# Kernel tuning notes

Hardware: AMD Instinct MI355X
Metric: run time of the kernel (lower is better)

Reference implementation:

```python
import jax, jax.numpy as jnp
import numpy as np

B, S, IN, E, H, FF, L = 8, 1024, 128, 512, 8, 2048, 4
HD = E // H
EPS = 1e-5


def make_pe(seq_len, d_model):
    position = np.arange(seq_len, dtype=np.float32)[:, None]
    div_term = np.exp(np.arange(0, d_model, 2, dtype=np.float32) * (-np.log(10000.0) / d_model))
    pe = np.zeros((seq_len, d_model), dtype=np.float32)
    pe[:, 0::2] = np.sin(position * div_term)
    pe[:, 1::2] = np.cos(position * div_term)
    return jnp.asarray(pe)


def setup_inputs() -> dict:
    key = jax.random.key(0)
    ks = jax.random.split(key, 16)
    s = 0.02
    return {
        "src": jax.random.normal(ks[0], (B, S, IN), jnp.float32),
        "distances": jax.random.uniform(ks[1], (B, S, S), jnp.float32),
        "proj_w": jax.random.normal(ks[2], (E, IN), jnp.float32) * s,
        "proj_b": jnp.zeros((E,), jnp.float32),
        "bn_g": jnp.ones((E,), jnp.float32),
        "bn_b": jnp.zeros((E,), jnp.float32),
        "in_proj_w": jax.random.normal(ks[3], (3 * E, E), jnp.float32) * s,
        "in_proj_b": jnp.zeros((3 * E,), jnp.float32),
        "dist_scale": jnp.array(1.0, jnp.float32),
        "lin1_w": jax.random.normal(ks[4], (FF, E), jnp.float32) * s,
        "lin1_b": jnp.zeros((FF,), jnp.float32),
        "lin2_w": jax.random.normal(ks[5], (E, FF), jnp.float32) * s,
        "lin2_b": jnp.zeros((E,), jnp.float32),
        "n1_g": jnp.ones((E,), jnp.float32),
        "n1_b": jnp.zeros((E,), jnp.float32),
        "n2_g": jnp.ones((E,), jnp.float32),
        "n2_b": jnp.zeros((E,), jnp.float32),
    }


def layernorm(x, g, b):
    m = jnp.mean(x, axis=-1, keepdims=True)
    v = jnp.var(x, axis=-1, keepdims=True)
    return (x - m) * jax.lax.rsqrt(v + EPS) * g + b


def reference(src, distances, proj_w, proj_b, bn_g, bn_b, in_proj_w, in_proj_b,
              dist_scale, lin1_w, lin1_b, lin2_w, lin2_b, n1_g, n1_b, n2_g, n2_b):
    # input projection
    x = jnp.einsum('bsi,ei->bse', src, proj_w) + proj_b  # [B,S,E]
    # BatchNorm1d over flattened (B*S) dim, training-mode batch stats
    xf = x.reshape(-1, E)
    mu = jnp.mean(xf, axis=0)
    var = jnp.var(xf, axis=0)
    x = ((xf - mu) * jax.lax.rsqrt(var + EPS) * bn_g + bn_b).reshape(B, S, E)
    # positional encoding
    x = x + make_pe(S, E)[None]
    # distance bias (same for every layer)
    dmax = jnp.max(distances, axis=-1, keepdims=True)
    dist_bias = jnp.exp(dist_scale * (1.0 - distances / dmax))  # [B,S,S]
    scale = 1.0 / jnp.sqrt(jnp.float32(HD))
    # num_layers iterations of the SAME (shared-parameter) layer
    for _ in range(L):
        qkv = jnp.einsum('bse,fe->bsf', x, in_proj_w) + in_proj_b  # [B,S,3E]
        q, k, v = jnp.split(qkv, 3, axis=-1)
        q = q.reshape(B, S, H, HD).transpose(0, 2, 1, 3)
        k = k.reshape(B, S, H, HD).transpose(0, 2, 1, 3)
        scores = jnp.einsum('bhqd,bhkd->bhqk', q, k) * scale  # [B,H,S,S]
        attn = jax.nn.softmax(scores, axis=-1)
        avg_w = jnp.mean(attn, axis=1)  # head-averaged weights [B,S,S]
        w = avg_w * dist_bias
        w = w / jnp.sum(w, axis=-1, keepdims=True)
        # NOTE: original bmm uses raw layer input as value (no V/out projection)
        attn_out = jnp.einsum('bqk,bke->bqe', w, x)
        x = layernorm(x + attn_out, n1_g, n1_b)
        ff = jnp.einsum('bsf,ef->bse', jax.nn.relu(jnp.einsum('bse,fe->bsf', x, lin1_w) + lin1_b), lin2_w) + lin2_b
        x = layernorm(x + ff, n2_g, n2_b)
    return x
```

## Files before the change

kernel.cpp:

```cpp
#include <hip/hip_runtime.h>
#include <hip/hip_bf16.h>
#include <math.h>

#define Bz 8
#define Sz 1024
#define INz 128
#define Ez 512
#define Hz 8
#define HDz 64
#define FFz 2048
#define Lz 4
#define Nz (Bz*Sz)
#define EPSf 1e-5f

typedef __attribute__((ext_vector_type(8))) short short8;
typedef __attribute__((ext_vector_type(4))) float floatx4;
#define MFMA16(a,b,c) __builtin_amdgcn_mfma_f32_16x16x32_bf16(a,b,c,0,0,0)

typedef __hip_bfloat16 bf16;

__device__ inline float b2f(bf16 v) { return __bfloat162float(v); }
__device__ inline bf16 f2b(float v) { return __float2bfloat16(v); }

__device__ inline void gload16(const bf16* g, bf16* lds_base)
{
  __builtin_amdgcn_global_load_lds(
      (const __attribute__((address_space(1))) void*)g,
      (__attribute__((address_space(3))) void*)lds_base,
      16, 0, 0);
}

__global__ __launch_bounds__(256) void cast_f2b(const float* __restrict__ in,
    bf16* __restrict__ out, int n)
{
  int i = blockIdx.x * 256 + threadIdx.x;
  if (i < n) out[i] = f2b(in[i]);
}

__global__ __launch_bounds__(256) void gemm_bt(
    const bf16* __restrict__ A, const bf16* __restrict__ Wm,
    const float* __restrict__ bias, float* __restrict__ Cf,
    bf16* __restrict__ Cb, const float* __restrict__ rowscale,
    int M, int N, int K, long sA, long sW, long sC, int relu)
{
  int z = blockIdx.z;
  A  += (size_t)z * sA;
  Wm += (size_t)z * sW;
  if (rowscale) rowscale += (size_t)z * M;
  size_t cbase = (size_t)z * sC;
  int bm = blockIdx.y * 128, bn = blockIdx.x * 128;
  __shared__ __align__(16) bf16 As[128][64];
  __shared__ __align__(16) bf16 Bs[128][64];
  int t = threadIdx.x, wave = t >> 6, lane = t & 63;
  int wm = (wave >> 1) * 64, wn = (wave & 1) * 64;
  int fr = lane & 15, fo = (lane >> 4) * 8;
  int srow = lane >> 3, scol = (lane & 7) * 8;
  floatx4 acc[4][4];
  #pragma unroll
  for (int i = 0; i < 4; ++i)
    #pragma unroll
    for (int j = 0; j < 4; ++j) acc[i][j] = (floatx4){0.f, 0.f, 0.f, 0.f};

  for (int k0 = 0; k0 < K; k0 += 64) {
    #pragma unroll
    for (int i = 0; i < 4; ++i) {
      int chunk = wave * 4 + i;
      int row = chunk * 8 + srow;
      gload16(A  + (size_t)(bm + row) * K + k0 + scol, &As[chunk * 8][0]);
      gload16(Wm + (size_t)(bn + row) * K + k0 + scol, &Bs[chunk * 8][0]);
    }
    __syncthreads();
    #pragma unroll
    for (int ks = 0; ks < 2; ++ks) {
      short8 af[4], bfv[4];
      #pragma unroll
      for (int rt = 0; rt < 4; ++rt) af[rt]  = *(const short8*)&As[wm + rt * 16 + fr][ks * 32 + fo];
      #pragma unroll
      for (int ct = 0; ct < 4; ++ct) bfv[ct] = *(const short8*)&Bs[wn + ct * 16 + fr][ks * 32 + fo];
      #pragma unroll
      for (int rt = 0; rt < 4; ++rt)
        #pragma unroll
        for (int ct = 0; ct < 4; ++ct)
          acc[rt][ct] = MFMA16(af[rt], bfv[ct], acc[rt][ct]);
    }
    __syncthreads();
  }
  #pragma unroll
  for (int rt = 0; rt < 4; ++rt) {
    #pragma unroll
    for (int r = 0; r < 4; ++r) {
      int row = bm + wm + rt * 16 + (lane >> 4) * 4 + r;
      float rs = rowscale ? (1.f / rowscale[row]) : 1.f;
      #pragma unroll
      for (int ct = 0; ct < 4; ++ct) {
        int col = bn + wn + ct * 16 + fr;
        float v = acc[rt][ct][r] + (bias ? bias[col] : 0.f);
        if (relu) v = fmaxf(v, 0.f);
        v *= rs;
        if (Cf) Cf[cbase + (size_t)row * N + col] = v;
        if (Cb) Cb[cbase + (size_t)row * N + col] = f2b(v);
      }
    }
  }
}

__global__ __launch_bounds__(256) void bn_stats(const float* __restrict__ x, float* __restrict__ st)
{
  int c = blockIdx.x;
  float s = 0.f, q = 0.f;
  for (int r = threadIdx.x; r < Nz; r += 256) {
    float v = x[(size_t)r * Ez + c];
    s += v; q += v * v;
  }
  for (int o = 32; o; o >>= 1) { s += __shfl_down(s, o); q += __shfl_down(q, o); }
  __shared__ float shs[4], shq[4];
  int w = threadIdx.x >> 6;
  if ((threadIdx.x & 63) == 0) { shs[w] = s; shq[w] = q; }
  __syncthreads();
  if (threadIdx.x == 0) {
    s = shs[0] + shs[1] + shs[2] + shs[3];
    q = shq[0] + shq[1] + shq[2] + shq[3];
    float mu = s / (float)Nz;
    float var = q / (float)Nz - mu * mu;
    st[c] = mu;
    st[Ez + c] = rsqrtf(var + EPSf);
  }
}

__global__ __launch_bounds__(256) void bn_apply_pe(const float* __restrict__ x0,
    const float* __restrict__ st, const float* __restrict__ g,
    const float* __restrict__ b, float* __restrict__ x, bf16* __restrict__ xb)
{
  int idx = blockIdx.x * 256 + threadIdx.x;
  int c = idx & (Ez - 1);
  int r = idx >> 9;
  int s = r & (Sz - 1);
  float dt = expf((float)(c & ~1) * (-9.210340371976184f / (float)Ez));
  float ang = (float)s * dt;
  float pe = (c & 1) ? cosf(ang) : sinf(ang);
  float mu = st[c], rs = st[Ez + c];
  float v = (x0[idx] - mu) * rs * g[c] + b[c] + pe;
  x[idx] = v;
  xb[idx] = f2b(v);
}

__global__ __launch_bounds__(256) void dist_bias_k(const float* __restrict__ dist,
    const float* __restrict__ dsc, bf16* __restrict__ db)
{
  size_t base = (size_t)blockIdx.x * Sz;
  float m = -1e30f;
  for (int j = threadIdx.x; j < Sz; j += 256) m = fmaxf(m, dist[base + j]);
  for (int o = 32; o; o >>= 1) m = fmaxf(m, __shfl_down(m, o));
  __shared__ float sh[4];
  if ((threadIdx.x & 63) == 0) sh[threadIdx.x >> 6] = m;
  __syncthreads();
  m = fmaxf(fmaxf(sh[0], sh[1]), fmaxf(sh[2], sh[3]));
  float sc = dsc[0];
  float inv = 1.f / m;
  for (int j = threadIdx.x; j < Sz; j += 256)
    db[base + j] = f2b(expf(sc * (1.f - dist[base + j] * inv)));
}

__global__ __launch_bounds__(256) void transpose_xb(const bf16* __restrict__ xb,
    bf16* __restrict__ xT)
{
  int b = blockIdx.z, e0 = blockIdx.y * 32, s0 = blockIdx.x * 32;
  __shared__ bf16 T[32][40];
  int t = threadIdx.x, row = t >> 3, c = t & 7;
  *(ushort4*)&T[row][c * 4] = *(const ushort4*)(xb + (size_t)(b * Sz + s0 + row) * Ez + e0 + c * 4);
  __syncthreads();
  ushort4 v;
  unsigned short* vp = (unsigned short*)&v;
  #pragma unroll
  for (int i = 0; i < 4; ++i) vp[i] = *(const unsigned short*)&T[c * 4 + i][row];
  *(ushort4*)(xT + ((size_t)b * Ez + e0 + row) * Sz + s0 + c * 4) = v;
}

__global__ __launch_bounds__(256) void attn_stats2(const bf16* __restrict__ qk,
    float* __restrict__ stats)
{
  int qt = blockIdx.x, h = blockIdx.y, b = blockIdx.z;
  int q0 = qt * 64;
  __shared__ bf16 Qs[64][72];
  __shared__ bf16 Ks[128][72];
  int t = threadIdx.x, wave = t >> 6, lane = t & 63;
  int fr = lane & 15, fo = (lane >> 4) * 8;
  #pragma unroll
  for (int i = 0; i < 2; ++i) {
    int idx = i * 256 + t, row = idx >> 3, c4 = idx & 7;
    *(float4*)&Qs[row][c4 * 8] =
      *(const float4*)(qk + (size_t)(b * Sz + q0 + row) * 1024 + h * 64 + c4 * 8);
  }
  __syncthreads();
  short8 aq0 = *(const short8*)&Qs[wave * 16 + fr][fo];
  short8 aq1 = *(const short8*)&Qs[wave * 16 + fr][32 + fo];
  float m_run[4] = {-1e30f, -1e30f, -1e30f, -1e30f};
  float z_run[4] = {0.f, 0.f, 0.f, 0.f};
  for (int k0 = 0; k0 < Sz; k0 += 128) {
    __syncthreads();
    #pragma unroll
    for (int i = 0; i < 4; ++i) {
      int idx = i * 256 + t, row = idx >> 3, c4 = idx & 7;
      *(float4*)&Ks[row][c4 * 8] =
        *(const float4*)(qk + (size_t)(b * Sz + k0 + row) * 1024 + 512 + h * 64 + c4 * 8);
    }
    __syncthreads();
    float sc[8][4];
    #pragma unroll
    for (int j = 0; j < 8; ++j) {
      floatx4 a4 = (floatx4){0.f, 0.f, 0.f, 0.f};
      short8 b0 = *(const short8*)&Ks[j * 16 + fr][fo];
      short8 b1 = *(const short8*)&Ks[j * 16 + fr][32 + fo];
      a4 = MFMA16(aq0, b0, a4);
      a4 = MFMA16(aq1, b1, a4);
      #pragma unroll
      for (int r = 0; r < 4; ++r) sc[j][r] = a4[r] * 0.125f;
    }
    #pragma unroll
    for (int r = 0; r < 4; ++r) {
      float vm = sc[0][r];
      #pragma unroll
      for (int j = 1; j < 8; ++j) vm = fmaxf(vm, sc[j][r]);
      #pragma unroll
      for (int o = 1; o < 16; o <<= 1) vm = fmaxf(vm, __shfl_xor(vm, o, 16));
      float mn = fmaxf(m_run[r], vm);
      float zb = 0.f;
      #pragma unroll
      for (int j = 0; j < 8; ++j) zb += __expf(sc[j][r] - mn);
      #pragma unroll
      for (int o = 1; o < 16; o <<= 1) zb += __shfl_xor(zb, o, 16);
      z_run[r] = z_run[r] * __expf(m_run[r] - mn) + zb;
      m_run[r] = mn;
    }
  }
  if (fr == 0) {
    int qb = q0 + wave * 16 + (lane >> 4) * 4;
    #pragma unroll
    for (int r = 0; r < 4; ++r) {
      size_t o = ((size_t)(b * Hz + h) * Sz + qb + r) * 2;
      stats[o] = m_run[r];
      stats[o + 1] = z_run[r];
    }
  }
}

__global__ __launch_bounds__(256) void scores_bias(const bf16* __restrict__ qk,
    const bf16* __restrict__ db, const float* __restrict__ stats,
    bf16* __restrict__ aw)
{
  int kt = blockIdx.x, qt = blockIdx.y, b = blockIdx.z;
  int q0 = qt * 128, k0 = kt * 128;
  __shared__ bf16 Qs[128][72];
  __shared__ bf16 Ks[128][72];
  __shared__ float mS[128][9];
  __shared__ float ziS[128][9];
  int t = threadIdx.x, wave = t >> 6, lane = t & 63;
  int fr = lane & 15, fo = (lane >> 4) * 8;
  int wm = (wave >> 1) * 64, wn = (wave & 1) * 64;

  #pragma unroll
  for (int i = 0; i < 4; ++i) {
    int lin = i * 256 + t, h = lin >> 7, q = lin & 127;
    const float* sp = stats + ((size_t)(b * Hz + h) * Sz + q0 + q) * 2;
    mS[q][h] = sp[0];
    ziS[q][h] = 1.f / sp[1];
  }

  floatx4 pac[4][4];
  #pragma unroll
  for (int i = 0; i < 4; ++i)
    #pragma unroll
    for (int j = 0; j < 4; ++j) pac[i][j] = (floatx4){0.f, 0.f, 0.f, 0.f};

  for (int h = 0; h < 8; ++h) {
    __syncthreads();
    #pragma unroll
    for (int i = 0; i < 4; ++i) {
      int idx = i * 256 + t, row = idx >> 3, c4 = idx & 7;
      *(float4*)&Qs[row][c4 * 8] =
        *(const float4*)(qk + (size_t)(b * Sz + q0 + row) * 1024 + h * 64 + c4 * 8);
      *(float4*)&Ks[row][c4 * 8] =
        *(const float4*)(qk + (size_t)(b * Sz + k0 + row) * 1024 + 512 + h * 64 + c4 * 8);
    }
    __syncthreads();
    short8 bfv0[4], bfv1[4];
    #pragma unroll
    for (int ct = 0; ct < 4; ++ct) {
      bfv0[ct] = *(const short8*)&Ks[wn + ct * 16 + fr][fo];
      bfv1[ct] = *(const short8*)&Ks[wn + ct * 16 + fr][32 + fo];
    }
    #pragma unroll
    for (int rt = 0; rt < 4; ++rt) {
      short8 af0 = *(const short8*)&Qs[wm + rt * 16 + fr][fo];
      short8 af1 = *(const short8*)&Qs[wm + rt * 16 + fr][32 + fo];
      floatx4 sc[4];
      #pragma unroll
      for (int ct = 0; ct < 4; ++ct) {
        floatx4 z4 = (floatx4){0.f, 0.f, 0.f, 0.f};
        z4 = MFMA16(af0, bfv0[ct], z4);
        sc[ct] = MFMA16(af1, bfv1[ct], z4);
      }
      #pragma unroll
      for (int r = 0; r < 4; ++r) {
        int qloc = wm + rt * 16 + (lane >> 4) * 4 + r;
        float m = mS[qloc][h], zi = ziS[qloc][h];
        #pragma unroll
        for (int ct = 0; ct < 4; ++ct)
          pac[rt][ct][r] += __expf(sc[ct][r] * 0.125f - m) * zi;
      }
    }
  }

  #pragma unroll
  for (int rt = 0; rt < 4; ++rt) {
    #pragma unroll
    for (int r = 0; r < 4; ++r) {
      int qloc = wm + rt * 16 + (lane >> 4) * 4 + r;
      size_t rowoff = (size_t)(b * Sz + q0 + qloc) * Sz + k0;
      #pragma unroll
      for (int ct = 0; ct < 4; ++ct) {
        int kloc = wn + ct * 16 + fr;
        float p = pac[rt][ct][r] * 0.125f * b2f(db[rowoff + kloc]);
        aw[rowoff + kloc] = f2b(p);
      }
    }
  }
}

__global__ __launch_bounds__(256) void rowsum(const bf16* __restrict__ aw,
    float* __restrict__ den)
{
  size_t base = (size_t)blockIdx.x * Sz;
  int t = threadIdx.x;
  ushort4 u = *(const ushort4*)(aw + base + t * 4);
  float s = __uint_as_float((unsigned)u.x << 16) + __uint_as_float((unsigned)u.y << 16)
          + __uint_as_float((unsigned)u.z << 16) + __uint_as_float((unsigned)u.w << 16);
  for (int o = 32; o; o >>= 1) s += __shfl_down(s, o);
  __shared__ float sh[4];
  if ((t & 63) == 0) sh[t >> 6] = s;
  __syncthreads();
  if (t == 0) den[blockIdx.x] = sh[0] + sh[1] + sh[2] + sh[3];
}

__global__ __launch_bounds__(256) void add_ln(const float* __restrict__ xin,
    const float* __restrict__ dly, const float* __restrict__ g,
    const float* __restrict__ bb, float* __restrict__ xout, bf16* __restrict__ xbout)
{
  size_t base = (size_t)blockIdx.x * Ez;
  int t = threadIdx.x;
  float a0 = xin[base + t] + dly[base + t];
  float a1 = xin[base + t + 256] + dly[base + t + 256];
  float s = a0 + a1, q = a0 * a0 + a1 * a1;
  for (int o = 32; o; o >>= 1) { s += __shfl_down(s, o); q += __shfl_down(q, o); }
  __shared__ float shs[4], shq[4];
  if ((t & 63) == 0) { shs[t >> 6] = s; shq[t >> 6] = q; }
  __syncthreads();
  s = shs[0] + shs[1] + shs[2] + shs[3];
  q = shq[0] + shq[1] + shq[2] + shq[3];
  float mu = s * (1.f / Ez);
  float var = q * (1.f / Ez) - mu * mu;
  float rs = rsqrtf(var + EPSf);
  float v0 = (a0 - mu) * rs * g[t] + bb[t];
  float v1 = (a1 - mu) * rs * g[t + 256] + bb[t + 256];
  xout[base + t] = v0;
  xout[base + t + 256] = v1;
  xbout[base + t] = f2b(v0);
  xbout[base + t + 256] = f2b(v1);
}

extern "C" void kernel_launch(void* const* d_in, const int* in_sizes, int n_in,
                              void* d_out, int out_size, void* d_ws, size_t ws_size,
                              hipStream_t stream)
{
  const float* src        = (const float*)d_in[0];
  const float* distances  = (const float*)d_in[1];
  const float* proj_w     = (const float*)d_in[2];
  const float* proj_b     = (const float*)d_in[3];
  const float* bn_g       = (const float*)d_in[4];
  const float* bn_b       = (const float*)d_in[5];
  const float* in_proj_w  = (const float*)d_in[6];
  const float* in_proj_b  = (const float*)d_in[7];
  const float* dist_scale = (const float*)d_in[8];
  const float* lin1_w     = (const float*)d_in[9];
  const float* lin1_b     = (const float*)d_in[10];
  const float* lin2_w     = (const float*)d_in[11];
  const float* lin2_b     = (const float*)d_in[12];
  const float* n1_g       = (const float*)d_in[13];
  const float* n1_b       = (const float*)d_in[14];
  const float* n2_g       = (const float*)d_in[15];
  const float* n2_b       = (const float*)d_in[16];

  float* x = (float*)d_out;

  float* stats = (float*)d_ws;
  float* den   = stats + 131072;
  float* bnst  = den + 8192;
  float* aout  = bnst + 1024;
  float* x0    = aout;
  bf16* db_b = (bf16*)(aout + (size_t)Nz * Ez);
  bf16* Rqk  = db_b + (size_t)Bz * Sz * Sz;
  bf16* qk   = Rqk;
  bf16* aw   = Rqk + (size_t)Nz * 1024;
  bf16* ff1  = Rqk;
  bf16* xb   = Rqk + (size_t)Nz * FFz;
  bf16* xT   = xb + (size_t)Nz * Ez;
  bf16* srcb = xT + (size_t)Bz * Ez * Sz;
  bf16* wpr  = srcb + (size_t)Nz * INz;
  bf16* wqk  = wpr + Ez * INz;
  bf16* wl1  = wqk + 1024 * Ez;
  bf16* wl2  = wl1 + FFz * Ez;

  cast_f2b<<<(Nz * INz) / 256, 256, 0, stream>>>(src, srcb, Nz * INz);
  cast_f2b<<<(Ez * INz + 255) / 256, 256, 0, stream>>>(proj_w, wpr, Ez * INz);
  cast_f2b<<<(1024 * Ez) / 256, 256, 0, stream>>>(in_proj_w, wqk, 1024 * Ez);
  cast_f2b<<<(FFz * Ez) / 256, 256, 0, stream>>>(lin1_w, wl1, FFz * Ez);
  cast_f2b<<<(Ez * FFz) / 256, 256, 0, stream>>>(lin2_w, wl2, Ez * FFz);

  gemm_bt<<<dim3(Ez / 128, Nz / 128, 1), 256, 0, stream>>>(
      srcb, wpr, proj_b, x0, nullptr, nullptr, Nz, Ez, INz, 0, 0, 0, 0);
  bn_stats<<<Ez, 256, 0, stream>>>(x0, bnst);
  bn_apply_pe<<<(Nz * Ez) / 256, 256, 0, stream>>>(x0, bnst, bn_g, bn_b, x, xb);
  dist_bias_k<<<Bz * Sz, 256, 0, stream>>>(distances, dist_scale, db_b);

  for (int l = 0; l < Lz; ++l) {
    transpose_xb<<<dim3(Sz / 32, Ez / 32, Bz), 256, 0, stream>>>(xb, xT);
    gemm_bt<<<dim3(1024 / 128, Nz / 128, 1), 256, 0, stream>>>(
        xb, wqk, in_proj_b, nullptr, qk, nullptr, Nz, 1024, Ez, 0, 0, 0, 0);
    attn_stats2<<<dim3(Sz / 64, Hz, Bz), 256, 0, stream>>>(qk, stats);
    scores_bias<<<dim3(Sz / 128, Sz / 128, Bz), 256, 0, stream>>>(qk, db_b, stats, aw);
    rowsum<<<Bz * Sz, 256, 0, stream>>>(aw, den);
    gemm_bt<<<dim3(Ez / 128, Sz / 128, Bz), 256, 0, stream>>>(
        aw, xT, nullptr, aout, nullptr, den,
        Sz, Ez, Sz, (long)Sz * Sz, (long)Ez * Sz, (long)Sz * Ez, 0);
    add_ln<<<Nz, 256, 0, stream>>>(x, aout, n1_g, n1_b, x, xb);
    gemm_bt<<<dim3(FFz / 128, Nz / 128, 1), 256, 0, stream>>>(
        xb, wl1, lin1_b, nullptr, ff1, nullptr, Nz, FFz, Ez, 0, 0, 0, 1);
    gemm_bt<<<dim3(Ez / 128, Nz / 128, 1), 256, 0, stream>>>(
        ff1, wl2, lin2_b, aout, nullptr, nullptr, Nz, Ez, FFz, 0, 0, 0, 0);
    add_ln<<<Nz, 256, 0, stream>>>(x, aout, n2_g, n2_b, x, xb);
  }
}
```

Before: 1.282 ms.

## Double-buffer LDS tiles and XOR-swizzle layout in bf16 GEMM

The GEMM kernel now uses two LDS buffers, so the global-to-LDS load of the next K tile is issued before computing on the current one. This halves the barriers per K step and hides load latency. It also XOR-swizzles the 16-byte column chunks in LDS, both on store and on fragment read, to reduce bank conflicts. LDS use doubles to 64KB per block, which may lower occupancy.

```diff
diff --git a/kernel.cpp b/kernel.cpp
--- a/kernel.cpp
+++ b/kernel.cpp
@@ -49,42 +49,61 @@
   if (rowscale) rowscale += (size_t)z * M;
   size_t cbase = (size_t)z * sC;
   int bm = blockIdx.y * 128, bn = blockIdx.x * 128;
-  __shared__ __align__(16) bf16 As[128][64];
-  __shared__ __align__(16) bf16 Bs[128][64];
+  __shared__ __align__(16) bf16 As0[128][64], Bs0[128][64];
+  __shared__ __align__(16) bf16 As1[128][64], Bs1[128][64];
   int t = threadIdx.x, wave = t >> 6, lane = t & 63;
   int wm = (wave >> 1) * 64, wn = (wave & 1) * 64;
-  int fr = lane & 15, fo = (lane >> 4) * 8;
-  int srow = lane >> 3, scol = (lane & 7) * 8;
+  int fr = lane & 15, fo = lane >> 4;
+  int srow = lane >> 3;
+  int scol = ((lane & 7) ^ srow) * 8;
   floatx4 acc[4][4];
   #pragma unroll
   for (int i = 0; i < 4; ++i)
     #pragma unroll
     for (int j = 0; j < 4; ++j) acc[i][j] = (floatx4){0.f, 0.f, 0.f, 0.f};
 
-  for (int k0 = 0; k0 < K; k0 += 64) {
-    #pragma unroll
-    for (int i = 0; i < 4; ++i) {
-      int chunk = wave * 4 + i;
-      int row = chunk * 8 + srow;
-      gload16(A  + (size_t)(bm + row) * K + k0 + scol, &As[chunk * 8][0]);
-      gload16(Wm + (size_t)(bn + row) * K + k0 + scol, &Bs[chunk * 8][0]);
-    }
+  #define STAGE(Ad, Bd, kk) do {                                            \
+    _Pragma("unroll")                                                        \
+    for (int i_ = 0; i_ < 4; ++i_) {                                         \
+      int chunk_ = wave * 4 + i_;                                            \
+      int row_ = chunk_ * 8 + srow;                                          \
+      gload16(A  + (size_t)(bm + row_) * K + (kk) + scol, &Ad[chunk_ * 8][0]);\
+      gload16(Wm + (size_t)(bn + row_) * K + (kk) + scol, &Bd[chunk_ * 8][0]);\
+    } } while (0)
+
+  #define COMPUTE(Ad, Bd) do {                                               \
+    _Pragma("unroll")                                                        \
+    for (int ks_ = 0; ks_ < 2; ++ks_) {                                      \
+      int sw_ = ((ks_ * 4 + fo) ^ (fr & 7)) * 8;                             \
+      short8 af_[4], bf_[4];                                                 \
+      _Pragma("unroll")                                                      \
+      for (int rt_ = 0; rt_ < 4; ++rt_)                                      \
+        af_[rt_] = *(const short8*)&Ad[wm + rt_ * 16 + fr][sw_];             \
+      _Pragma("unroll")                                                      \
+      for (int ct_ = 0; ct_ < 4; ++ct_)                                      \
+        bf_[ct_] = *(const short8*)&Bd[wn + ct_ * 16 + fr][sw_];             \
+      _Pragma("unroll")                                                      \
+      for (int rt_ = 0; rt_ < 4; ++rt_)                                      \
+        _Pragma("unroll")                                                    \
+        for (int ct_ = 0; ct_ < 4; ++ct_)                                    \
+          acc[rt_][ct_] = MFMA16(af_[rt_], bf_[ct_], acc[rt_][ct_]);         \
+    } } while (0)
+
+  STAGE(As0, Bs0, 0);
+  __syncthreads();
+  for (int k0 = 0; k0 < K; k0 += 128) {
+    if (k0 + 64 < K) STAGE(As1, Bs1, k0 + 64);
+    COMPUTE(As0, Bs0);
     __syncthreads();
-    #pragma unroll
-    for (int ks = 0; ks < 2; ++ks) {
-      short8 af[4], bfv[4];
-      #pragma unroll
-      for (int rt = 0; rt < 4; ++rt) af[rt]  = *(const short8*)&As[wm + rt * 16 + fr][ks * 32 + fo];
-      #pragma unroll
-      for (int ct = 0; ct < 4; ++ct) bfv[ct] = *(const short8*)&Bs[wn + ct * 16 + fr][ks * 32 + fo];
-      #pragma unroll
-      for (int rt = 0; rt < 4; ++rt)
-        #pragma unroll
-        for (int ct = 0; ct < 4; ++ct)
-          acc[rt][ct] = MFMA16(af[rt], bfv[ct], acc[rt][ct]);
-    }
-    __syncthreads();
-  }
+    if (k0 + 64 < K) {
+      if (k0 + 128 < K) STAGE(As0, Bs0, k0 + 128);
+      COMPUTE(As1, Bs1);
+      __syncthreads();
+    }
+  }
+  #undef STAGE
+  #undef COMPUTE
+
   #pragma unroll
   for (int rt = 0; rt < 4; ++rt) {
     #pragma unroll
```

Result: faster. 1.181 ms (-7.9%).
